# Kernel tuning notes

Hardware: AMD Instinct MI355X
Metric: run time of the kernel (lower is better)

The kernel has to match this reference:

```python
import jax, jax.numpy as jnp
import numpy as np

B, T, C, H = 4, 2048, 1024, 16
D = C // H  # head dim = 64


def setup_inputs() -> dict:
    key = jax.random.key(0)
    k_x, k_wa, k_ba, k_wp, k_bp = jax.random.split(key, 5)
    s = 1.0 / np.sqrt(C)
    return {
        "x": jax.random.normal(k_x, (B, T, C), dtype=jnp.float32),
        "w_attn": jax.random.uniform(k_wa, (C, 3 * C), minval=-s, maxval=s, dtype=jnp.float32),
        "b_attn": jax.random.uniform(k_ba, (3 * C,), minval=-s, maxval=s, dtype=jnp.float32),
        "w_proj": jax.random.uniform(k_wp, (C, C), minval=-s, maxval=s, dtype=jnp.float32),
        "b_proj": jax.random.uniform(k_bp, (C,), minval=-s, maxval=s, dtype=jnp.float32),
    }


def reference(x, w_attn, b_attn, w_proj, b_proj):
    b, t, c = x.shape
    qkv = x @ w_attn + b_attn  # [b, t, 3c]
    q, k, v = jnp.split(qkv, 3, axis=-1)
    # [b, h, t, d]
    q = q.reshape(b, t, H, D).transpose(0, 2, 1, 3)
    k = k.reshape(b, t, H, D).transpose(0, 2, 1, 3)
    v = v.reshape(b, t, H, D).transpose(0, 2, 1, 3)
    scale = 1.0 / np.sqrt(D)
    logits = jnp.einsum("bhqd,bhkd->bhqk", q, k) * scale
    causal = jnp.tril(jnp.ones((t, t), dtype=bool))
    logits = jnp.where(causal, logits, jnp.finfo(logits.dtype).min)
    attn = jax.nn.softmax(logits, axis=-1)
    y = jnp.einsum("bhqk,bhkd->bhqd", attn, v)
    y = y.transpose(0, 2, 1, 3).reshape(b, t, c)
    return y @ w_proj + b_proj
```

## Files before the change

kernel.cpp:

```cpp
#include <hip/hip_runtime.h>


using u16 = unsigned short;
using u32 = unsigned int;
using bf16x8 = __attribute__((ext_vector_type(8))) __bf16;
using f32x4  = __attribute__((ext_vector_type(4))) float;
using f32x16 = __attribute__((ext_vector_type(16))) float;
using u16x8  = __attribute__((ext_vector_type(8))) u16;
using u16x4  = __attribute__((ext_vector_type(4))) u16;
using u32x2  = __attribute__((ext_vector_type(2))) u32;
using u32x4  = __attribute__((ext_vector_type(4))) u32;
using fvec4  = __attribute__((ext_vector_type(4))) float;

__device__ __forceinline__ u16 f2bf(float f) {
  u32 u = __builtin_bit_cast(u32, f);
  u32 r = (u + 0x7FFFu + ((u >> 16) & 1u)) >> 16;
  return (u16)r;
}

__device__ __forceinline__ u32 cvtpk(float lo, float hi) {
  u32 r;
  asm("v_cvt_pk_bf16_f32 %0, %1, %2" : "=v"(r) : "v"(lo), "v"(hi));
  return r;
}

__device__ __forceinline__ f32x4 mfma16(bf16x8 a, bf16x8 b, f32x4 c) {
  return __builtin_amdgcn_mfma_f32_16x16x32_bf16(a, b, c, 0, 0, 0);
}

__device__ __forceinline__ f32x16 mfma32(bf16x8 a, bf16x8 b, f32x16 c) {
  return __builtin_amdgcn_mfma_f32_32x32x16_bf16(a, b, c, 0, 0, 0);
}

__device__ __forceinline__ void gld16(const u16* g, u16* l) {
  __builtin_amdgcn_global_load_lds(
      (const __attribute__((address_space(1))) void*)g,
      (__attribute__((address_space(3))) void*)l, 16, 0, 0);
}

__global__ __launch_bounds__(256) void conv_kernel(
    const float* __restrict__ in, u16* __restrict__ out) {
  const size_t i = ((size_t)blockIdx.x * 256 + threadIdx.x) * 8;
  fvec4 a = *(const fvec4*)(in + i);
  fvec4 b = *(const fvec4*)(in + i + 4);
  u16x8 h;
#pragma unroll
  for (int j = 0; j < 4; ++j) { h[j] = f2bf(a[j]); h[4 + j] = f2bf(b[j]); }
  *(u16x8*)(out + i) = h;
}

__global__ __launch_bounds__(256) void transpose_conv_kernel(
    const float* __restrict__ W, u16* __restrict__ Wt, int K, int N) {
  __shared__ float tile[32][33];
  const int n0 = blockIdx.x * 32, k0 = blockIdx.y * 32;
  const int tx = threadIdx.x, ty = threadIdx.y;
#pragma unroll
  for (int j = 0; j < 4; ++j)
    tile[ty + j * 8][tx] = W[(size_t)(k0 + ty + j * 8) * N + n0 + tx];
  __syncthreads();
#pragma unroll
  for (int j = 0; j < 4; ++j)
    Wt[(size_t)(n0 + ty + j * 8) * K + k0 + tx] = f2bf(tile[tx][ty + j * 8]);
}

template <bool QKV>
__global__ __launch_bounds__(256) void gemm_kernel(
    const u16* __restrict__ A, const u16* __restrict__ Bt,
    const float* __restrict__ bias, void* __restrict__ Cp,
    u16* __restrict__ vt, int M, int N, int K) {
  constexpr float SC = 0.18033688011112042f;
  __shared__ u16 As[2][4096];
  __shared__ u16 Bs[2][4096];
  const int tid = threadIdx.x;
  const int l = tid & 63, w = tid >> 6;
  const int l15 = l & 15, l16 = l >> 4;
  const int wm = (w >> 1) * 64, wn = (w & 1) * 64;

  const u32 nwg = gridDim.x * gridDim.y;
  u32 f = blockIdx.y * gridDim.x + blockIdx.x;
  f = (f & 7) * (nwg >> 3) + (f >> 3);
  const long mbase = (long)(f / gridDim.x) * 128;
  const long nbase = (long)(f % gridDim.x) * 128;

  const int srow = tid >> 2;
  const int scol = ((tid & 3) ^ ((srow >> 1) & 3)) * 8;
  const u16* gA0 = A + (mbase + srow) * (long)K + scol;
  const u16* gA1 = gA0 + 64 * (long)K;
  const u16* gB0 = Bt + (nbase + srow) * (long)K + scol;
  const u16* gB1 = gB0 + 64 * (long)K;

  f32x4 acc[4][4] = {};
  const int NT = K >> 5;

#define STAGE(buf, koff)                         \
  gld16(gA0 + (koff), &As[buf][tid * 8]);        \
  gld16(gA1 + (koff), &As[buf][tid * 8 + 2048]); \
  gld16(gB0 + (koff), &Bs[buf][tid * 8]);        \
  gld16(gB1 + (koff), &Bs[buf][tid * 8 + 2048]);

  STAGE(0, 0);
  asm volatile("s_waitcnt vmcnt(0)" ::: "memory");
  __builtin_amdgcn_s_barrier();

  for (int t = 0; t < NT; ++t) {
    const int cur = t & 1;
    if (t + 1 < NT) { STAGE(cur ^ 1, (t + 1) * 32); }

    bf16x8 af[4], bfr[4];
#pragma unroll
    for (int i = 0; i < 4; ++i) {
      const int row = wm + i * 16 + l15;
      af[i] = *(const bf16x8*)(&As[cur][row * 32 + ((l16 ^ ((row >> 1) & 3)) * 8)]);
    }
#pragma unroll
    for (int j = 0; j < 4; ++j) {
      const int row = wn + j * 16 + l15;
      bfr[j] = *(const bf16x8*)(&Bs[cur][row * 32 + ((l16 ^ ((row >> 1) & 3)) * 8)]);
    }
    asm volatile("s_waitcnt lgkmcnt(0)" ::: "memory");
    __builtin_amdgcn_sched_barrier(0);
    __builtin_amdgcn_s_setprio(1);
#pragma unroll
    for (int i = 0; i < 4; ++i)
#pragma unroll
      for (int j = 0; j < 4; ++j)
        acc[i][j] = mfma16(af[i], bfr[j], acc[i][j]);
    __builtin_amdgcn_s_setprio(0);
    __builtin_amdgcn_sched_barrier(0);
    if (t + 1 < NT) { asm volatile("s_waitcnt vmcnt(0)" ::: "memory"); }
    __builtin_amdgcn_s_barrier();
  }
#undef STAGE

  if constexpr (QKV) {
    const bool isv = (nbase >= 2048);
#pragma unroll
    for (int i = 0; i < 4; ++i) {
#pragma unroll
      for (int j = 0; j < 4; ++j) {
        const long m0 = mbase + wm + i * 16 + l16 * 4;
        const int n = (int)nbase + wn + j * 16 + l15;
        const float bv = bias[n];
        if (!isv) {
          u16* qkp = (u16*)Cp;
          const float sc = (n < 1024) ? SC : 1.0f;
#pragma unroll
          for (int r = 0; r < 4; ++r)
            qkp[(m0 + r) * 2048 + n] = f2bf((acc[i][j][r] + bv) * sc);
        } else {
          const int vc = n - 2048, hh = vc >> 6, dd = vc & 63;
          const int bb = (int)(m0 >> 11), t0 = (int)(m0 & 2047);
          u16x4 pk;
#pragma unroll
          for (int r = 0; r < 4; ++r) pk[r] = f2bf(acc[i][j][r] + bv);
          *(u16x4*)(vt + ((size_t)(bb * 16 + hh) * 64 + dd) * 2048 + t0) = pk;
        }
      }
    }
  } else {
#pragma unroll
    for (int i = 0; i < 4; ++i) {
#pragma unroll
      for (int j = 0; j < 4; ++j) {
        const long row0 = mbase + wm + i * 16 + l16 * 4;
        const long col = nbase + wn + j * 16 + l15;
        const float bv = bias[col];
#pragma unroll
        for (int r = 0; r < 4; ++r)
          ((float*)Cp)[(row0 + r) * (long)N + col] = acc[i][j][r] + bv;
      }
    }
  }
}

__global__ __launch_bounds__(256, 2) void flash_kernel(
    const u16* __restrict__ qk, const u16* __restrict__ vt, u16* __restrict__ attn_out) {
  __shared__ u16 Ks[2][64 * 64];
  const int tid = threadIdx.x;
  const int lane = tid & 63, w = tid >> 6;
  const int l31 = lane & 31, hi = lane >> 5;
  const int xorv = (l31 & 7) << 4;

  const u32 i = blockIdx.y * 8 + blockIdx.x;
  const int jj = i >> 3;
  const int bh = (i & 7) | ((jj & 7) << 3);
  const int pair = (int)(i >> 6);
  const int b = bh >> 4, h = bh & 15;
  const u16* qbase = qk + (size_t)b * 2048 * 2048 + h * 64;
  const u16* kbase = qbase + 1024;
  const u16* vbase = vt + (size_t)bh * 64 * 2048;
  u16* obase = attn_out + (size_t)b * 2048 * 1024 + h * 64;

  const int srow = tid >> 3;
  const int sslot = (tid & 7) ^ (srow & 7);
  const u16* gk = kbase + (size_t)srow * 2048 + sslot * 8;

  int cur = 0;
  for (int half = 0; half < 2; ++half) {
    const int qt = half ? (15 - pair) : pair;
    const int nt = 2 * qt + 2;
    const int qr0 = qt * 128 + w * 32;
    const int q = qr0 + l31;

    bf16x8 qf[4];
#pragma unroll
    for (int ds = 0; ds < 4; ++ds)
      qf[ds] = *(const bf16x8*)(qbase + (size_t)q * 2048 + ds * 16 + hi * 8);

    f32x16 oacc[2] = {};
    float lsum = 0.f;

    gld16(gk, &Ks[cur][tid * 8]);
    gld16(gk + (size_t)32 * 2048, &Ks[cur][tid * 8 + 2048]);
    asm volatile("s_waitcnt vmcnt(0)" ::: "memory");
    __builtin_amdgcn_s_barrier();

    for (int kt = 0; kt < nt; ++kt) {
      const int kb = kt * 64;
      if (kt + 1 < nt) {
        gld16(gk + (size_t)(kb + 64) * 2048, &Ks[cur ^ 1][tid * 8]);
        gld16(gk + (size_t)(kb + 96) * 2048, &Ks[cur ^ 1][tid * 8 + 2048]);
      }
      u16x8 vf[2][4];
#pragma unroll
      for (int dh = 0; dh < 2; ++dh)
#pragma unroll
        for (int ks = 0; ks < 4; ++ks)
          vf[dh][ks] = *(const u16x8*)(vbase + (size_t)(dh * 32 + l31) * 2048 + kb + ks * 16 + hi * 8);

      f32x16 s0 = {}, s1 = {};
      __builtin_amdgcn_s_setprio(1);
#pragma unroll
      for (int ds = 0; ds < 4; ++ds) {
        const int col = (ds * 32 + hi * 16) ^ xorv;
        bf16x8 k0 = *(const bf16x8*)((const char*)&Ks[cur][0] + l31 * 128 + col);
        bf16x8 k1 = *(const bf16x8*)((const char*)&Ks[cur][0] + (32 + l31) * 128 + col);
        s0 = mfma32(k0, qf[ds], s0);
        s1 = mfma32(k1, qf[ds], s1);
      }
      __builtin_amdgcn_s_setprio(0);

      if (kb + 63 > qr0) {
#pragma unroll
        for (int r = 0; r < 16; ++r) {
          const int crow = (r & 3) + 8 * (r >> 2) + 4 * hi;
          if (kb + crow > q) s0[r] = -1e30f;
          if (kb + 32 + crow > q) s1[r] = -1e30f;
        }
      }

      float p0[16], p1[16];
      float ps = 0.f;
#pragma unroll
      for (int r = 0; r < 16; ++r) {
        p0[r] = exp2f(s0[r]);
        p1[r] = exp2f(s1[r]);
        ps += p0[r] + p1[r];
      }
      lsum += ps;

      bf16x8 pf[4];
#pragma unroll
      for (int kh = 0; kh < 2; ++kh) {
#pragma unroll
        for (int c = 0; c < 2; ++c) {
          const float* pp = kh ? p1 : p0;
          const int bs = c * 8;
          u32 L0 = cvtpk(pp[bs + 0], pp[bs + 1]);
          u32 L1 = cvtpk(pp[bs + 2], pp[bs + 3]);
          u32 L2 = cvtpk(pp[bs + 4], pp[bs + 5]);
          u32 L3 = cvtpk(pp[bs + 6], pp[bs + 7]);
          asm("v_permlane32_swap_b32 %0, %1" : "+v"(L0), "+v"(L2));
          asm("v_permlane32_swap_b32 %0, %1" : "+v"(L1), "+v"(L3));
          u32x4 pk = {L0, L1, L2, L3};
          pf[kh * 2 + c] = __builtin_bit_cast(bf16x8, pk);
        }
      }

      __builtin_amdgcn_s_setprio(1);
#pragma unroll
      for (int dh = 0; dh < 2; ++dh)
#pragma unroll
        for (int ks = 0; ks < 4; ++ks)
          oacc[dh] = mfma32(__builtin_bit_cast(bf16x8, vf[dh][ks]), pf[ks], oacc[dh]);
      __builtin_amdgcn_s_setprio(0);

      asm volatile("s_waitcnt vmcnt(0)" ::: "memory");
      __builtin_amdgcn_s_barrier();
      cur ^= 1;
    }

    lsum += __shfl_xor(lsum, 32);
    const float inv = 1.0f / lsum;
    u16* orow = obase + (size_t)q * 1024;
#pragma unroll
    for (int dh = 0; dh < 2; ++dh) {
#pragma unroll
      for (int jq = 0; jq < 4; ++jq) {
        u32x2 pk;
        pk[0] = cvtpk(oacc[dh][jq * 4 + 0] * inv, oacc[dh][jq * 4 + 1] * inv);
        pk[1] = cvtpk(oacc[dh][jq * 4 + 2] * inv, oacc[dh][jq * 4 + 3] * inv);
        *(u32x2*)(orow + dh * 32 + 8 * jq + 4 * hi) = pk;
      }
    }
  }
}

extern "C" void kernel_launch(void* const* d_in, const int* in_sizes, int n_in,
                              void* d_out, int out_size, void* d_ws, size_t ws_size,
                              hipStream_t stream) {
  (void)in_sizes; (void)n_in; (void)out_size; (void)ws_size;
  const float* x      = (const float*)d_in[0];
  const float* w_attn = (const float*)d_in[1];
  const float* b_attn = (const float*)d_in[2];
  const float* w_proj = (const float*)d_in[3];
  const float* b_proj = (const float*)d_in[4];
  float* out = (float*)d_out;

  char* ws = (char*)d_ws;
  u16* qkbuf = (u16*)(ws);
  u16* vtbuf = (u16*)(ws + 33554432);
  u16* xbf   = (u16*)(ws + 50331648);
  u16* attnb = (u16*)(ws + 50331648);
  u16* wtA   = (u16*)(ws + 67108864);
  u16* wtP   = (u16*)(ws + 73400320);

  conv_kernel<<<4096, 256, 0, stream>>>(x, xbf);
  transpose_conv_kernel<<<dim3(3072 / 32, 1024 / 32), dim3(32, 8), 0, stream>>>(w_attn, wtA, 1024, 3072);
  transpose_conv_kernel<<<dim3(1024 / 32, 1024 / 32), dim3(32, 8), 0, stream>>>(w_proj, wtP, 1024, 1024);

  gemm_kernel<true><<<dim3(3072 / 128, 8192 / 128), 256, 0, stream>>>(
      xbf, wtA, b_attn, qkbuf, vtbuf, 8192, 3072, 1024);

  flash_kernel<<<dim3(8, 64), 256, 0, stream>>>(qkbuf, vtbuf, attnb);

  gemm_kernel<false><<<dim3(1024 / 128, 8192 / 128), 256, 0, stream>>>(
      attnb, wtP, b_proj, out, nullptr, 8192, 1024, 1024);
}
```

Before: 203.4 us.

## Use 2-wave flash blocks with 64 query rows per wave and LDS-staged V

Result: no change. 201.4 us (-0.9%).

```diff
diff --git a/kernel.cpp b/kernel.cpp
--- a/kernel.cpp
+++ b/kernel.cpp
@@ -173,9 +173,10 @@
   }
 }
 
-__global__ __launch_bounds__(256, 2) void flash_kernel(
+__global__ __launch_bounds__(128, 1) void flash_kernel(
     const u16* __restrict__ qk, const u16* __restrict__ vt, u16* __restrict__ attn_out) {
   __shared__ u16 Ks[2][64 * 64];
+  __shared__ u16 Vs[2][64 * 64];
   const int tid = threadIdx.x;
   const int lane = tid & 63, w = tid >> 6;
   const int l31 = lane & 31, hi = lane >> 5;
@@ -191,98 +192,119 @@
   const u16* vbase = vt + (size_t)bh * 64 * 2048;
   u16* obase = attn_out + (size_t)b * 2048 * 1024 + h * 64;
 
-  const int srow = tid >> 3;
-  const int sslot = (tid & 7) ^ (srow & 7);
-  const u16* gk = kbase + (size_t)srow * 2048 + sslot * 8;
+  const int sr = tid >> 3;
+  const int ss = (tid & 7) ^ (sr & 7);
+  const u16* gk = kbase + (size_t)sr * 2048 + ss * 8;
+  const u16* gv = vbase + (size_t)sr * 2048 + ss * 8;
+  const int dofs = tid * 8;
 
   int cur = 0;
   for (int half = 0; half < 2; ++half) {
     const int qt = half ? (15 - pair) : pair;
     const int nt = 2 * qt + 2;
-    const int qr0 = qt * 128 + w * 32;
-    const int q = qr0 + l31;
-
-    bf16x8 qf[4];
-#pragma unroll
-    for (int ds = 0; ds < 4; ++ds)
-      qf[ds] = *(const bf16x8*)(qbase + (size_t)q * 2048 + ds * 16 + hi * 8);
-
-    f32x16 oacc[2] = {};
-    float lsum = 0.f;
-
-    gld16(gk, &Ks[cur][tid * 8]);
-    gld16(gk + (size_t)32 * 2048, &Ks[cur][tid * 8 + 2048]);
+    const int qr0 = qt * 128 + w * 64;
+
+    bf16x8 qf[2][4];
+#pragma unroll
+    for (int g = 0; g < 2; ++g)
+#pragma unroll
+      for (int ds = 0; ds < 4; ++ds)
+        qf[g][ds] = *(const bf16x8*)(qbase + (size_t)(qr0 + g * 32 + l31) * 2048 + ds * 16 + hi * 8);
+
+    f32x16 oaccA[2] = {}, oaccB[2] = {};
+    float lsumA = 0.f, lsumB = 0.f;
+
+#pragma unroll
+    for (int j = 0; j < 4; ++j) {
+      gld16(gk + (size_t)(j * 16) * 2048, &Ks[cur][j * 1024 + dofs]);
+      gld16(gv + (size_t)(j * 16) * 2048, &Vs[cur][j * 1024 + dofs]);
+    }
     asm volatile("s_waitcnt vmcnt(0)" ::: "memory");
     __builtin_amdgcn_s_barrier();
 
     for (int kt = 0; kt < nt; ++kt) {
       const int kb = kt * 64;
       if (kt + 1 < nt) {
-        gld16(gk + (size_t)(kb + 64) * 2048, &Ks[cur ^ 1][tid * 8]);
-        gld16(gk + (size_t)(kb + 96) * 2048, &Ks[cur ^ 1][tid * 8 + 2048]);
-      }
-      u16x8 vf[2][4];
-#pragma unroll
-      for (int dh = 0; dh < 2; ++dh)
-#pragma unroll
-        for (int ks = 0; ks < 4; ++ks)
-          vf[dh][ks] = *(const u16x8*)(vbase + (size_t)(dh * 32 + l31) * 2048 + kb + ks * 16 + hi * 8);
-
-      f32x16 s0 = {}, s1 = {};
+#pragma unroll
+        for (int j = 0; j < 4; ++j) {
+          gld16(gk + (size_t)(kb + 64 + j * 16) * 2048, &Ks[cur ^ 1][j * 1024 + dofs]);
+          gld16(gv + (size_t)(j * 16) * 2048 + (kb + 64), &Vs[cur ^ 1][j * 1024 + dofs]);
+        }
+      }
+
+      bf16x8 pfA[4], pfB[4];
+#pragma unroll
+      for (int kh = 0; kh < 2; ++kh) {
+        f32x16 sA = {}, sB = {};
+        __builtin_amdgcn_s_setprio(1);
+#pragma unroll
+        for (int ds = 0; ds < 4; ++ds) {
+          const int row = kh * 32 + l31;
+          bf16x8 kf = *(const bf16x8*)((const char*)&Ks[cur][0] + row * 128 + ((ds * 32 + hi * 16) ^ xorv));
+          sA = mfma32(kf, qf[0][ds], sA);
+          sB = mfma32(kf, qf[1][ds], sB);
+        }
+        __builtin_amdgcn_s_setprio(0);
+
+        if (kb + kh * 32 + 31 > qr0) {
+#pragma unroll
+          for (int r = 0; r < 16; ++r) {
+            const int key = kb + kh * 32 + (r & 3) + 8 * (r >> 2) + 4 * hi;
+            if (key > qr0 + l31) sA[r] = -1e30f;
+            if (key > qr0 + 32 + l31) sB[r] = -1e30f;
+          }
+        }
+
+        float psA = 0.f, psB = 0.f;
+#pragma unroll
+        for (int r = 0; r < 16; ++r) {
+          sA[r] = exp2f(sA[r]); psA += sA[r];
+          sB[r] = exp2f(sB[r]); psB += sB[r];
+        }
+        lsumA += psA; lsumB += psB;
+
+#pragma unroll
+        for (int c = 0; c < 2; ++c) {
+          const int bs = c * 8;
+          {
+            u32 L0 = cvtpk(sA[bs + 0], sA[bs + 1]);
+            u32 L1 = cvtpk(sA[bs + 2], sA[bs + 3]);
+            u32 L2 = cvtpk(sA[bs + 4], sA[bs + 5]);
+            u32 L3 = cvtpk(sA[bs + 6], sA[bs + 7]);
+            asm("v_permlane32_swap_b32 %0, %1" : "+v"(L0), "+v"(L2));
+            asm("v_permlane32_swap_b32 %0, %1" : "+v"(L1), "+v"(L3));
+            u32x4 pk = {L0, L1, L2, L3};
+            pfA[kh * 2 + c] = __builtin_bit_cast(bf16x8, pk);
+          }
+          {
+            u32 L0 = cvtpk(sB[bs + 0], sB[bs + 1]);
+            u32 L1 = cvtpk(sB[bs + 2], sB[bs + 3]);
+            u32 L2 = cvtpk(sB[bs + 4], sB[bs + 5]);
+            u32 L3 = cvtpk(sB[bs + 6], sB[bs + 7]);
+            asm("v_permlane32_swap_b32 %0, %1" : "+v"(L0), "+v"(L2));
+            asm("v_permlane32_swap_b32 %0, %1" : "+v"(L1), "+v"(L3));
+            u32x4 pk = {L0, L1, L2, L3};
+            pfB[kh * 2 + c] = __builtin_bit_cast(bf16x8, pk);
+          }
+        }
+      }
+
       __builtin_amdgcn_s_setprio(1);
 #pragma unroll
-      for (int ds = 0; ds < 4; ++ds) {
-        const int col = (ds * 32 + hi * 16) ^ xorv;
-        bf16x8 k0 = *(const bf16x8*)((const char*)&Ks[cur][0] + l31 * 128 + col);
-        bf16x8 k1 = *(const bf16x8*)((const char*)&Ks[cur][0] + (32 + l31) * 128 + col);
-        s0 = mfma32(k0, qf[ds], s0);
-        s1 = mfma32(k1, qf[ds], s1);
-      }
-      __builtin_amdgcn_s_setprio(0);
-
-      if (kb + 63 > qr0) {
-#pragma unroll
-        for (int r = 0; r < 16; ++r) {
-          const int crow = (r & 3) + 8 * (r >> 2) + 4 * hi;
-          if (kb + crow > q) s0[r] = -1e30f;
-          if (kb + 32 + crow > q) s1[r] = -1e30f;
-        }
-      }
-
-      float p0[16], p1[16];
-      float ps = 0.f;
-#pragma unroll
-      for (int r = 0; r < 16; ++r) {
-        p0[r] = exp2f(s0[r]);
-        p1[r] = exp2f(s1[r]);
-        ps += p0[r] + p1[r];
-      }
-      lsum += ps;
-
-      bf16x8 pf[4];
-#pragma unroll
-      for (int kh = 0; kh < 2; ++kh) {
-#pragma unroll
-        for (int c = 0; c < 2; ++c) {
-          const float* pp = kh ? p1 : p0;
-          const int bs = c * 8;
-          u32 L0 = cvtpk(pp[bs + 0], pp[bs + 1]);
-          u32 L1 = cvtpk(pp[bs + 2], pp[bs + 3]);
-          u32 L2 = cvtpk(pp[bs + 4], pp[bs + 5]);
-          u32 L3 = cvtpk(pp[bs + 6], pp[bs + 7]);
-          asm("v_permlane32_swap_b32 %0, %1" : "+v"(L0), "+v"(L2));
-          asm("v_permlane32_swap_b32 %0, %1" : "+v"(L1), "+v"(L3));
-          u32x4 pk = {L0, L1, L2, L3};
-          pf[kh * 2 + c] = __builtin_bit_cast(bf16x8, pk);
-        }
-      }
-
-      __builtin_amdgcn_s_setprio(1);
-#pragma unroll
-      for (int dh = 0; dh < 2; ++dh)
-#pragma unroll
-        for (int ks = 0; ks < 4; ++ks)
-          oacc[dh] = mfma32(__builtin_bit_cast(bf16x8, vf[dh][ks]), pf[ks], oacc[dh]);
+      for (int dh = 0; dh < 2; ++dh) {
+#pragma unroll
+        for (int ks = 0; ks < 4; ++ks) {
+          const int row = dh * 32 + l31;
+          bf16x8 vf = *(const bf16x8*)((const char*)&Vs[cur][0] + row * 128 + ((ks * 32 + hi * 16) ^ xorv));
+          if (dh == 0) {
+            oaccA[0] = mfma32(vf, pfA[ks], oaccA[0]);
+            oaccB[0] = mfma32(vf, pfB[ks], oaccB[0]);
+          } else {
+            oaccA[1] = mfma32(vf, pfA[ks], oaccA[1]);
+            oaccB[1] = mfma32(vf, pfB[ks], oaccB[1]);
+          }
+        }
+      }
       __builtin_amdgcn_s_setprio(0);
 
       asm volatile("s_waitcnt vmcnt(0)" ::: "memory");
@@ -290,17 +312,22 @@
       cur ^= 1;
     }
 
-    lsum += __shfl_xor(lsum, 32);
-    const float inv = 1.0f / lsum;
-    u16* orow = obase + (size_t)q * 1024;
-#pragma unroll
-    for (int dh = 0; dh < 2; ++dh) {
-#pragma unroll
-      for (int jq = 0; jq < 4; ++jq) {
-        u32x2 pk;
-        pk[0] = cvtpk(oacc[dh][jq * 4 + 0] * inv, oacc[dh][jq * 4 + 1] * inv);
-        pk[1] = cvtpk(oacc[dh][jq * 4 + 2] * inv, oacc[dh][jq * 4 + 3] * inv);
-        *(u32x2*)(orow + dh * 32 + 8 * jq + 4 * hi) = pk;
+#pragma unroll
+    for (int g = 0; g < 2; ++g) {
+      float ls = g ? lsumB : lsumA;
+      ls += __shfl_xor(ls, 32);
+      const float inv = 1.0f / ls;
+      u16* orow = obase + (size_t)(qr0 + g * 32 + l31) * 1024;
+#pragma unroll
+      for (int dh = 0; dh < 2; ++dh) {
+        const f32x16& oa = g ? oaccB[dh] : oaccA[dh];
+#pragma unroll
+        for (int jq = 0; jq < 4; ++jq) {
+          u32x2 pk;
+          pk[0] = cvtpk(oa[jq * 4 + 0] * inv, oa[jq * 4 + 1] * inv);
+          pk[1] = cvtpk(oa[jq * 4 + 2] * inv, oa[jq * 4 + 3] * inv);
+          *(u32x2*)(orow + dh * 32 + 8 * jq + 4 * hi) = pk;
+        }
       }
     }
   }
@@ -332,7 +359,7 @@
   gemm_kernel<true><<<dim3(3072 / 128, 8192 / 128), 256, 0, stream>>>(
       xbf, wtA, b_attn, qkbuf, vtbuf, 8192, 3072, 1024);
 
-  flash_kernel<<<dim3(8, 64), 256, 0, stream>>>(qkbuf, vtbuf, attnb);
+  flash_kernel<<<dim3(8, 64), 128, 0, stream>>>(qkbuf, vtbuf, attnb);
 
   gemm_kernel<false><<<dim3(1024 / 128, 8192 / 128), 256, 0, stream>>>(
       attnb, wtP, b_proj, out, nullptr, 8192, 1024, 1024);
```
